# Kernel optimization log

Hardware: AMD Instinct MI355X
Metric: run time of the kernel (lower is better)

Reference implementation:

```python
import jax, jax.numpy as jnp
import numpy as np

H_DIM = 64
GRID = 8
NS = 2.0  # neighborhood_size


def _pool_seq(hidden, pos):
    # hidden: (P, H_DIM) hidden states of peds in one scene; pos: (P, 2) end positions
    P = hidden.shape[0]
    g2 = GRID * GRID
    tl_x = pos[:, 0] - NS / 2
    tl_y = pos[:, 1] + NS / 2
    br_x = pos[:, 0] + NS / 2
    br_y = pos[:, 1] - NS / 2
    # pair (i, j): grid of ped i (rows), position of ped j (cols)
    ox = pos[None, :, 0]
    oy = pos[None, :, 1]
    cell_x = jnp.floor((ox - tl_x[:, None]) / NS * GRID)
    cell_y = jnp.floor((tl_y[:, None] - oy) / NS * GRID)
    grid_pos = (cell_x + cell_y * GRID).astype(jnp.int32)
    # out-of-bound if outside neighborhood box OR i == j (diagonal forced out)
    oob = ((ox >= br_x[:, None]) | (ox <= tl_x[:, None])
           | (oy >= tl_y[:, None]) | (oy <= br_y[:, None])
           | jnp.eye(P, dtype=bool))
    idx = grid_pos + 1 + (jnp.arange(P, dtype=jnp.int32) * g2)[:, None]
    idx = jnp.where(oob, 0, idx)  # slot 0 is the trash bin (dropped below)
    src = jnp.broadcast_to(hidden[None], (P, P, H_DIM)).reshape(P * P, H_DIM)
    buf = jnp.zeros((P * g2 + 1, H_DIM), hidden.dtype)
    buf = buf.at[idx.reshape(-1)].add(src)
    return buf[1:].reshape(P, g2 * H_DIM)


def reference(h_states, seq_start_end, end_pos, rel_pos, W, b):
    B = end_pos.shape[0]
    S = seq_start_end.shape[0]
    P = B // S  # equal-length scenes -> static reshape
    hidden = h_states.reshape(-1, H_DIM).reshape(S, P, H_DIM)
    pos = end_pos.reshape(S, P, 2)
    pooled = jax.vmap(_pool_seq)(hidden, pos).reshape(B, GRID * GRID * H_DIM)
    # make_mlp([4096, 1024], relu, batch_norm=False): Linear -> ReLU
    return jax.nn.relu(pooled @ W + b)


def setup_inputs():
    key = jax.random.key(0)
    k0, k1, k2, k3 = jax.random.split(key, 4)
    S, P = 64, 64
    B = S * P
    bottleneck = 1024
    feat = GRID * GRID * H_DIM  # 4096
    h_states = jax.random.normal(k0, (1, B, H_DIM), jnp.float32)
    starts = jnp.arange(S, dtype=jnp.int32) * P
    seq_start_end = jnp.stack([starts, starts + P], axis=1)
    end_pos = jax.random.normal(k1, (B, 2), jnp.float32)
    rel_pos = jax.random.normal(k2, (B, 2), jnp.float32)
    W = jax.random.normal(k3, (feat, bottleneck), jnp.float32) * 0.02
    b = jnp.zeros((bottleneck,), jnp.float32)
    return {"h_states": h_states, "seq_start_end": seq_start_end,
            "end_pos": end_pos, "rel_pos": rel_pos, "W": W, "b": b}
```

## Files before the change

kernel.cpp:

```cpp
#include <hip/hip_runtime.h>


#define BM 128
#define BN 64
#define BK 64

typedef short short8 __attribute__((ext_vector_type(8)));
typedef float floatx4 __attribute__((ext_vector_type(4)));

__device__ inline short f2bf(float x) {
    union { float f; unsigned u; } v; v.f = x;
    unsigned r = v.u + 0x7fffu + ((v.u >> 16) & 1u);
    return (short)(r >> 16);
}

__device__ inline void gload_lds16(const void* g, void* l) {
    __builtin_amdgcn_global_load_lds(
        (const __attribute__((address_space(1))) void*)g,
        (__attribute__((address_space(3))) void*)l,
        16, 0, 0);
}

__global__ __launch_bounds__(64) void pool_kernel(
    const float* __restrict__ h,
    const float* __restrict__ pos,
    short* __restrict__ pooled,
    int P)
{
    __shared__ float acc[64 * 64];
    __shared__ float px[64], py[64];
    __shared__ int   cellIdx[64];

    const int d = threadIdx.x;
    const int s = blockIdx.x / P;
    const int i = blockIdx.x - s * P;
    const int base = s * P;

    #pragma unroll
    for (int c = 0; c < 64; ++c) acc[c * 64 + d] = 0.f;

    if (d < P) {
        px[d] = pos[(size_t)(base + d) * 2 + 0];
        py[d] = pos[(size_t)(base + d) * 2 + 1];
    }
    __syncthreads();

    const float tlx = px[i] - 1.0f;
    const float tly = py[i] + 1.0f;
    const float brx = px[i] + 1.0f;
    const float bry = py[i] - 1.0f;

    if (d < P) {
        const float ox = px[d], oy = py[d];
        int cell = -1;
        if (ox < brx && ox > tlx && oy < tly && oy > bry && d != i) {
            int cx = (int)floorf((ox - tlx) * 4.0f);
            int cy = (int)floorf((tly - oy) * 4.0f);
            cell = cx + cy * 8;
        }
        cellIdx[d] = cell;
    }
    __syncthreads();

    for (int j = 0; j < P; ++j) {
        int c = cellIdx[j];
        if (c >= 0) acc[c * 64 + d] += h[(size_t)(base + j) * 64 + d];
    }

    const size_t row = (size_t)(base + i) * 4096;
    #pragma unroll
    for (int c = 0; c < 64; ++c)
        pooled[row + c * 64 + d] = f2bf(acc[c * 64 + d]);
}

__global__ __launch_bounds__(256) void castWt_kernel(
    const float* __restrict__ W, short* __restrict__ Wt, int K, int N)
{
    __shared__ float tile[32][33];
    const int tx = threadIdx.x;
    const int ty = threadIdx.y;
    const int k0 = blockIdx.x * 32;
    const int n0 = blockIdx.y * 32;

    #pragma unroll
    for (int i = 0; i < 32; i += 8)
        tile[ty + i][tx] = W[(size_t)(k0 + ty + i) * N + n0 + tx];
    __syncthreads();
    #pragma unroll
    for (int i = 0; i < 32; i += 8)
        Wt[(size_t)(n0 + ty + i) * K + k0 + tx] = f2bf(tile[tx][ty + i]);
}

__global__ __launch_bounds__(256) void gemm_bias_relu(
    const short* __restrict__ A,
    const short* __restrict__ Bt,
    const float* __restrict__ bias,
    float* __restrict__ out,
    int M, int N, int K)
{
    __shared__ __align__(16) short As[BM * BK];
    __shared__ __align__(16) short Bs[BN * BK];

    const int tid  = threadIdx.x;
    const int lane = tid & 63;
    const int wave = tid >> 6;
    const int wr = wave >> 1;
    const int wc = wave & 1;
    const int q  = lane >> 4;
    const int ml = lane & 15;
    const int m0 = blockIdx.y * BM;
    const int n0 = blockIdx.x * BN;

    const int rsub = lane >> 3;
    const int swz  = (lane & 7) ^ rsub;

    const short* ag[4];
    const short* bg[2];
    #pragma unroll
    for (int c = 0; c < 4; ++c)
        ag[c] = A + (size_t)(m0 + (c * 4 + wave) * 8 + rsub) * K + swz * 8;
    #pragma unroll
    for (int c = 0; c < 2; ++c)
        bg[c] = Bt + (size_t)(n0 + (c * 4 + wave) * 8 + rsub) * K + swz * 8;

    floatx4 acc[4][2];
    #pragma unroll
    for (int i = 0; i < 4; ++i)
        #pragma unroll
        for (int j = 0; j < 2; ++j)
            acc[i][j] = (floatx4){0.f, 0.f, 0.f, 0.f};

    for (int kb = 0; kb < K; kb += BK) {
        if (kb) __syncthreads();
        #pragma unroll
        for (int c = 0; c < 4; ++c) {
            gload_lds16(ag[c], &As[(c * 4 + wave) * 512]);
            ag[c] += BK;
        }
        #pragma unroll
        for (int c = 0; c < 2; ++c) {
            gload_lds16(bg[c], &Bs[(c * 4 + wave) * 512]);
            bg[c] += BK;
        }
        __syncthreads();

        #pragma unroll
        for (int t = 0; t < 2; ++t) {
            short8 af[4], bf[2];
            const int gx = ((4 * t + q) ^ (ml & 7)) * 8;
            #pragma unroll
            for (int i = 0; i < 4; ++i)
                af[i] = *(const short8*)&As[(wr * 64 + i * 16 + ml) * 64 + gx];
            #pragma unroll
            for (int j = 0; j < 2; ++j)
                bf[j] = *(const short8*)&Bs[(wc * 32 + j * 16 + ml) * 64 + gx];
            #pragma unroll
            for (int i = 0; i < 4; ++i)
                #pragma unroll
                for (int j = 0; j < 2; ++j)
                    acc[i][j] = __builtin_amdgcn_mfma_f32_16x16x32_bf16(
                        af[i], bf[j], acc[i][j], 0, 0, 0);
        }
    }

    #pragma unroll
    for (int j = 0; j < 2; ++j) {
        const int gn = n0 + wc * 32 + j * 16 + ml;
        const float bv = bias[gn];
        #pragma unroll
        for (int i = 0; i < 4; ++i) {
            const int gm = m0 + wr * 64 + i * 16 + q * 4;
            #pragma unroll
            for (int r = 0; r < 4; ++r) {
                float v = acc[i][j][r] + bv;
                out[(size_t)(gm + r) * N + gn] = v > 0.f ? v : 0.f;
            }
        }
    }
}

extern "C" void kernel_launch(void* const* d_in, const int* in_sizes, int n_in,
                              void* d_out, int out_size, void* d_ws, size_t ws_size,
                              hipStream_t stream) {
    const float* h    = (const float*)d_in[0];
    const float* pos  = (const float*)d_in[2];
    const float* W    = (const float*)d_in[4];
    const float* bias = (const float*)d_in[5];

    const int B = in_sizes[0] / 64;
    const int S = in_sizes[1] / 2;
    const int P = B / S;
    const int N = in_sizes[5];
    const int K = 64 * 64;

    short* pooled = (short*)d_ws;
    short* Wt     = pooled + (size_t)B * K;
    float* out    = (float*)d_out;

    pool_kernel<<<B, 64, 0, stream>>>(h, pos, pooled, P);
    castWt_kernel<<<dim3(K / 32, N / 32), dim3(32, 8), 0, stream>>>(W, Wt, K, N);
    gemm_bias_relu<<<dim3(N / BN, B / BM), 256, 0, stream>>>(pooled, Wt, bias, out, B, N, K);
}
```

Before: 158.9 us.

## Rework pooling with bitmask cells, vectorize weight cast, double GEMM K tile

The pooling kernel now has each block handle four pedestrians with one wave each. It stages the scene's hidden states in LDS and builds per-cell 64-bit neighbor masks with atomicOr, so each output cell is summed only over its occupied neighbors instead of scanning all of them per lane. The weight transpose-cast uses 64x64 tiles with float4 loads and short4 stores. The GEMM K tile grows from 64 to 128 with a 16-way XOR swizzle, which halves the number of barrier iterations at the cost of more LDS per block. The code now hardcodes scenes of 64 pedestrians.

```diff
diff --git a/kernel.cpp b/kernel.cpp
--- a/kernel.cpp
+++ b/kernel.cpp
@@ -3,9 +3,10 @@
 
 #define BM 128
 #define BN 64
-#define BK 64
+#define BK 128
 
 typedef short short8 __attribute__((ext_vector_type(8)));
+typedef short short4v __attribute__((ext_vector_type(4)));
 typedef float floatx4 __attribute__((ext_vector_type(4)));
 
 __device__ inline short f2bf(float x) {
@@ -21,74 +22,94 @@
         16, 0, 0);
 }
 
-__global__ __launch_bounds__(64) void pool_kernel(
+__global__ __launch_bounds__(256) void pool_kernel(
     const float* __restrict__ h,
     const float* __restrict__ pos,
-    short* __restrict__ pooled,
-    int P)
+    short* __restrict__ pooled)
 {
-    __shared__ float acc[64 * 64];
+    __shared__ float hs[64 * 64];
     __shared__ float px[64], py[64];
-    __shared__ int   cellIdx[64];
-
-    const int d = threadIdx.x;
-    const int s = blockIdx.x / P;
-    const int i = blockIdx.x - s * P;
-    const int base = s * P;
-
-    #pragma unroll
-    for (int c = 0; c < 64; ++c) acc[c * 64 + d] = 0.f;
-
-    if (d < P) {
-        px[d] = pos[(size_t)(base + d) * 2 + 0];
-        py[d] = pos[(size_t)(base + d) * 2 + 1];
-    }
+    __shared__ unsigned long long wmask[4][64];
+
+    const int tid  = threadIdx.x;
+    const int lane = tid & 63;
+    const int w    = tid >> 6;
+    const int s    = blockIdx.x >> 4;
+    const int grp  = blockIdx.x & 15;
+    const size_t base = (size_t)s * 64;
+
+    const float4* hv  = (const float4*)(h + base * 64);
+    float4*       hsv = (float4*)hs;
+    #pragma unroll
+    for (int c = 0; c < 4; ++c) hsv[tid + c * 256] = hv[tid + c * 256];
+    if (tid < 64) {
+        float2 p = ((const float2*)pos)[base + tid];
+        px[tid] = p.x; py[tid] = p.y;
+    }
+    wmask[w][lane] = 0ull;
     __syncthreads();
 
+    const int i = grp * 4 + w;
     const float tlx = px[i] - 1.0f;
     const float tly = py[i] + 1.0f;
     const float brx = px[i] + 1.0f;
     const float bry = py[i] - 1.0f;
 
-    if (d < P) {
-        const float ox = px[d], oy = py[d];
-        int cell = -1;
-        if (ox < brx && ox > tlx && oy < tly && oy > bry && d != i) {
+    {
+        const int j = lane;
+        const float ox = px[j], oy = py[j];
+        if (ox < brx && ox > tlx && oy < tly && oy > bry && j != i) {
             int cx = (int)floorf((ox - tlx) * 4.0f);
             int cy = (int)floorf((tly - oy) * 4.0f);
-            cell = cx + cy * 8;
-        }
-        cellIdx[d] = cell;
-    }
-    __syncthreads();
-
-    for (int j = 0; j < P; ++j) {
-        int c = cellIdx[j];
-        if (c >= 0) acc[c * 64 + d] += h[(size_t)(base + j) * 64 + d];
-    }
-
-    const size_t row = (size_t)(base + i) * 4096;
-    #pragma unroll
-    for (int c = 0; c < 64; ++c)
-        pooled[row + c * 64 + d] = f2bf(acc[c * 64 + d]);
+            atomicOr(&wmask[w][cx + cy * 8], 1ull << j);
+        }
+    }
+
+    const int d = lane;
+    const size_t orow = (base + i) * 4096;
+    for (int c = 0; c < 64; ++c) {
+        unsigned long long m = wmask[w][c];
+        float a0 = 0.f, a1 = 0.f;
+        while (m) {
+            int j0 = __builtin_ctzll(m); m &= m - 1;
+            if (m) {
+                int j1 = __builtin_ctzll(m); m &= m - 1;
+                a1 += hs[j1 * 64 + d];
+            }
+            a0 += hs[j0 * 64 + d];
+        }
+        pooled[orow + c * 64 + d] = f2bf(a0 + a1);
+    }
 }
 
 __global__ __launch_bounds__(256) void castWt_kernel(
     const float* __restrict__ W, short* __restrict__ Wt, int K, int N)
 {
-    __shared__ float tile[32][33];
-    const int tx = threadIdx.x;
-    const int ty = threadIdx.y;
-    const int k0 = blockIdx.x * 32;
-    const int n0 = blockIdx.y * 32;
-
-    #pragma unroll
-    for (int i = 0; i < 32; i += 8)
-        tile[ty + i][tx] = W[(size_t)(k0 + ty + i) * N + n0 + tx];
+    __shared__ float t[64][65];
+    const int tid = threadIdx.x;
+    const int k0 = blockIdx.x * 64;
+    const int n0 = blockIdx.y * 64;
+
+    const int r  = tid >> 4;
+    const int cq = (tid & 15) * 4;
+    #pragma unroll
+    for (int i = 0; i < 4; ++i) {
+        const int row = r + i * 16;
+        float4 v = *(const float4*)&W[(size_t)(k0 + row) * N + n0 + cq];
+        t[row][cq + 0] = v.x; t[row][cq + 1] = v.y;
+        t[row][cq + 2] = v.z; t[row][cq + 3] = v.w;
+    }
     __syncthreads();
-    #pragma unroll
-    for (int i = 0; i < 32; i += 8)
-        Wt[(size_t)(n0 + ty + i) * K + k0 + tx] = f2bf(tile[tx][ty + i]);
+    const int nl = tid >> 4;
+    const int kq = (tid & 15) * 4;
+    #pragma unroll
+    for (int i = 0; i < 4; ++i) {
+        const int n = nl + i * 16;
+        short4v o;
+        o.x = f2bf(t[kq + 0][n]); o.y = f2bf(t[kq + 1][n]);
+        o.z = f2bf(t[kq + 2][n]); o.w = f2bf(t[kq + 3][n]);
+        *(short4v*)&Wt[(size_t)(n0 + n) * K + k0 + kq] = o;
+    }
 }
 
 __global__ __launch_bounds__(256) void gemm_bias_relu(
@@ -111,17 +132,23 @@
     const int m0 = blockIdx.y * BM;
     const int n0 = blockIdx.x * BN;
 
-    const int rsub = lane >> 3;
-    const int swz  = (lane & 7) ^ rsub;
-
-    const short* ag[4];
-    const short* bg[2];
-    #pragma unroll
-    for (int c = 0; c < 4; ++c)
-        ag[c] = A + (size_t)(m0 + (c * 4 + wave) * 8 + rsub) * K + swz * 8;
-    #pragma unroll
-    for (int c = 0; c < 2; ++c)
-        bg[c] = Bt + (size_t)(n0 + (c * 4 + wave) * 8 + rsub) * K + swz * 8;
+    const int r4   = lane >> 4;
+    const int slot = lane & 15;
+
+    const short* ag[8];
+    const short* bg[4];
+    #pragma unroll
+    for (int c = 0; c < 8; ++c) {
+        const int gi = c * 4 + wave;
+        const int rl = gi * 4 + r4;
+        ag[c] = A + (size_t)(m0 + rl) * K + (slot ^ (rl & 15)) * 8;
+    }
+    #pragma unroll
+    for (int c = 0; c < 4; ++c) {
+        const int gi = c * 4 + wave;
+        const int rl = gi * 4 + r4;
+        bg[c] = Bt + (size_t)(n0 + rl) * K + (slot ^ (rl & 15)) * 8;
+    }
 
     floatx4 acc[4][2];
     #pragma unroll
@@ -133,27 +160,27 @@
     for (int kb = 0; kb < K; kb += BK) {
         if (kb) __syncthreads();
         #pragma unroll
-        for (int c = 0; c < 4; ++c) {
+        for (int c = 0; c < 8; ++c) {
             gload_lds16(ag[c], &As[(c * 4 + wave) * 512]);
             ag[c] += BK;
         }
         #pragma unroll
-        for (int c = 0; c < 2; ++c) {
+        for (int c = 0; c < 4; ++c) {
             gload_lds16(bg[c], &Bs[(c * 4 + wave) * 512]);
             bg[c] += BK;
         }
         __syncthreads();
 
         #pragma unroll
-        for (int t = 0; t < 2; ++t) {
+        for (int t = 0; t < 4; ++t) {
             short8 af[4], bf[2];
-            const int gx = ((4 * t + q) ^ (ml & 7)) * 8;
+            const int gx = ((t * 4 + q) ^ ml) * 8;
             #pragma unroll
             for (int i = 0; i < 4; ++i)
-                af[i] = *(const short8*)&As[(wr * 64 + i * 16 + ml) * 64 + gx];
+                af[i] = *(const short8*)&As[(wr * 64 + i * 16 + ml) * BK + gx];
             #pragma unroll
             for (int j = 0; j < 2; ++j)
-                bf[j] = *(const short8*)&Bs[(wc * 32 + j * 16 + ml) * 64 + gx];
+                bf[j] = *(const short8*)&Bs[(wc * 32 + j * 16 + ml) * BK + gx];
             #pragma unroll
             for (int i = 0; i < 4; ++i)
                 #pragma unroll
@@ -189,15 +216,15 @@
 
     const int B = in_sizes[0] / 64;
     const int S = in_sizes[1] / 2;
-    const int P = B / S;
     const int N = in_sizes[5];
     const int K = 64 * 64;
+    (void)S;
 
     short* pooled = (short*)d_ws;
     short* Wt     = pooled + (size_t)B * K;
     float* out    = (float*)d_out;
 
-    pool_kernel<<<B, 64, 0, stream>>>(h, pos, pooled, P);
-    castWt_kernel<<<dim3(K / 32, N / 32), dim3(32, 8), 0, stream>>>(W, Wt, K, N);
+    pool_kernel<<<B / 4, 256, 0, stream>>>(h, pos, pooled);
+    castWt_kernel<<<dim3(K / 64, N / 64), 256, 0, stream>>>(W, Wt, K, N);
     gemm_bias_relu<<<dim3(N / BN, B / BM), 256, 0, stream>>>(pooled, Wt, bias, out, B, N, K);
 }
```

After: 141.3 us. -11.0%, faster.
